# Performance work log

Measured on AMD Instinct MI355X. Metric: run time of the kernel, lower is better.

## Reference

```python
import jax, jax.numpy as jnp
import numpy as np
import math

B, H, M, L, D = 4, 8, 512, 2048, 64   # batch, heads, block len, span, head dim
RAMP = 64                              # adapt_span_len (soft-mask ramp size)


def setup_inputs() -> dict:
    key = jax.random.key(0)
    ks = jax.random.split(key, 5)
    BH = B * H
    KL = M + L
    return {
        "query": jax.random.normal(ks[0], (BH, M, D), jnp.float32),
        "key_": jax.random.normal(ks[1], (BH, KL, D), jnp.float32),
        "value": jax.random.normal(ks[2], (BH, KL, D), jnp.float32),
        "key_pe": jax.random.normal(ks[3], (1, D, L), jnp.float32) * 0.02,
        "current_val": jax.random.uniform(ks[4], (H, 1, 1), jnp.float32, minval=0.3, maxval=0.9),
    }


def reference(query, key_, value, key_pe, current_val):
    BH, Mq, Dh = query.shape
    KL = key_.shape[1]
    Lw = KL - Mq  # attention span
    nb = BH // current_val.shape[0]  # batch size (heads folded into leading dim)

    # full scores then unskew: band[b, i, j] = scores[b, i, i + j]
    scores = jnp.einsum('bmd,bnd->bmn', query, key_)              # (BH, M, M+L)
    rows = jnp.arange(Mq)[:, None]                                # (M, 1)
    band_idx = rows + jnp.arange(Lw)[None, :]                     # (M, L)
    attn = scores[:, rows, band_idx]                              # (BH, M, L)

    # relative position bias, scale, softmax
    attn = attn + jnp.einsum('bmd,dl->bml', query, key_pe[0])
    attn = attn / math.sqrt(Dh)
    attn = jax.nn.softmax(attn, axis=-1)

    # adaptive span soft mask (per head) + renormalization
    template = jnp.arange(1 - Lw, 1, dtype=attn.dtype)            # (L,) = linspace(1-L, 0, L)
    mask = jnp.clip((template + current_val * Lw) / RAMP + 1.0, 0.0, 1.0)  # (H, 1, L)
    attn4 = attn.reshape(nb, -1, Mq, Lw) * mask[None]             # (B, H, M, L)
    attn4 = attn4 / (attn4.sum(-1, keepdims=True) + 1e-8)
    attn = attn4.reshape(BH, Mq, Lw)

    # skew back to (BH, M, M+L) and contract with values
    skewed = jnp.zeros((BH, Mq, KL), attn.dtype).at[:, rows, band_idx].set(attn)
    out = jnp.einsum('bmn,bnd->bmd', skewed, value)               # (BH, M, D)
    return out
```

## Files before the change

### kernel.cpp

```cpp
#include <hip/hip_runtime.h>

typedef _Float16 half_t;
typedef _Float16 half8 __attribute__((ext_vector_type(8)));
typedef _Float16 half4 __attribute__((ext_vector_type(4)));
typedef float f32x4 __attribute__((ext_vector_type(4)));

#define MFMA32(a, b, c) __builtin_amdgcn_mfma_f32_16x16x32_f16((a), (b), (c), 0, 0, 0)
#define MFMA16(a, b, c) __builtin_amdgcn_mfma_f32_16x16x16f16((a), (b), (c), 0, 0, 0)

static constexpr int kM  = 512;
static constexpr int kD  = 64;
static constexpr int kKL = 2560;
static constexpr int kL  = 2048;
static constexpr int WS_QS  = 0;
static constexpr int WS_KB  = 1048576;
static constexpr int WS_VC  = WS_KB + 5242880;
static constexpr int WS_PET = WS_VC + 5242880;
static constexpr int WS_Z   = WS_PET + 131072;

__global__ __launch_bounds__(256) void prep_kernel(const float* __restrict__ q,
    const float* __restrict__ k, const float* __restrict__ v,
    const float* __restrict__ pe, half_t* __restrict__ ws, float* __restrict__ out) {
  __shared__ float ls[64 * 72];
  const int b = blockIdx.x, t = threadIdx.x;
  if (b < 3072) {
    const int i = b * 256 + t;
    const float QS = 0.125f * 1.4426950408889634f;
    const float* src; half_t* dst; float sc;
    if (i < 131072) { src = q + (size_t)i * 8; dst = ws + WS_QS + (size_t)i * 8; sc = QS; }
    else { const int j = i - 131072; src = k + (size_t)j * 8; dst = ws + WS_KB + (size_t)j * 8; sc = 1.0f; }
    const float4 a = ((const float4*)src)[0];
    const float4 bb = ((const float4*)src)[1];
    half_t tt[8];
    tt[0] = (half_t)(a.x * sc);  tt[1] = (half_t)(a.y * sc);
    tt[2] = (half_t)(a.z * sc);  tt[3] = (half_t)(a.w * sc);
    tt[4] = (half_t)(bb.x * sc); tt[5] = (half_t)(bb.y * sc);
    tt[6] = (half_t)(bb.z * sc); tt[7] = (half_t)(bb.w * sc);
    *(int4*)dst = *(int4*)tt;
    return;
  }
  if (b >= 4384) {
    if (b < 4640) {
      float4* o = (float4*)out;
      const int base = (b - 4384) * 1024 + t;
#pragma unroll
      for (int u = 0; u < 4; ++u) o[base + u * 256] = float4{0, 0, 0, 0};
    } else {
      float4* z = (float4*)((float*)(ws + WS_Z));
      const int base = (b - 4640) * 1024 + t;
#pragma unroll
      for (int u = 0; u < 4; ++u) z[base + u * 256] = float4{0, 0, 0, 0};
    }
    return;
  }
  const bool isV = (b < 4352);
  int bh = 0, kt = 0, b3 = 0;
  const float* src; int sstride;
  if (isV) {
    const int b2 = b - 3072;
    bh = b2 / 40; kt = b2 % 40;
    src = v + (size_t)(bh * 2560 + kt * 64) * 64; sstride = 64;
  } else {
    b3 = b - 4352;
    src = pe + (size_t)b3 * 64; sstride = 2048;
  }
  const int rr = t >> 4, cq = (t & 15) * 4;
#pragma unroll
  for (int p = 0; p < 4; ++p) {
    const float4 x = *(const float4*)(src + (size_t)(p * 16 + rr) * sstride + cq);
    *(float4*)(ls + (p * 16 + rr) * 72 + cq) = x;
  }
  __syncthreads();
  const int oc = t >> 2, ch = t & 3;
  half_t tmp[16];
#pragma unroll
  for (int i2 = 0; i2 < 16; ++i2) tmp[i2] = (half_t)ls[(ch * 16 + i2) * 72 + oc];
  half_t* o;
  if (isV) {
    o = ws + WS_VC + (size_t)bh * 163840 + ((kt << 1) + (ch >> 1)) * 2048 + oc * 32 + ((ch & 1) << 4);
  } else {
    o = ws + WS_PET + ((size_t)b3 * 64 + oc) * 64 + ch * 16;
  }
  ((int4*)o)[0] = ((int4*)tmp)[0];
  ((int4*)o)[1] = ((int4*)tmp)[1];
}

__global__ __launch_bounds__(256, 3) void attn_kernel(
    const half_t* __restrict__ ws, const float* __restrict__ cvp,
    float* __restrict__ out, float* __restrict__ zmA) {

  __shared__ __align__(16) char smem[36864];
  half_t* lsh = (half_t*)smem;

  const int tid  = threadIdx.x;
  const int lane = tid & 63;
  const int w    = tid >> 6;
  const int c    = lane & 15;
  const int qd   = lane >> 4;

  const int id = blockIdx.x;
  const int bh = ((id & 7) << 2) | (id >> 8);
  const int mid = (id >> 3) & 31;
  const int mb = mid & 3, sp = mid >> 2;
  const int m0 = mb << 7;
  const int g0   = (sp < 4) ? sp * 9 : 36 + (sp - 4) * 8;
  const int tmax = (sp < 4) ? 9 : 8;

  const float cvl = cvp[bh & 7] * 2048.0f - 2047.0f;
  const float cvO = cvl * 0.015625f + 1.0f;

  const half_t* kb  = ws + WS_KB + (size_t)bh * (kKL * kD);
  const half_t* vcb = ws + WS_VC + (size_t)bh * (kKL * kD);
  const half_t* pet = ws + WS_PET;

  half8 bq0[2], bq1[2];
#pragma unroll
  for (int f = 0; f < 2; ++f) {
    const half_t* qrow = ws + WS_QS + (size_t)(bh * kM + m0 + 32 * w + 16 * f + c) * kD;
    bq0[f] = *(const half8*)(qrow + qd * 8);
    bq1[f] = *(const half8*)(qrow + 32 + qd * 8);
  }

  int4 stgK, stgV;
  auto issueKV = [&](int gg) {
    const int r = tid >> 3, seg = tid & 7;
    const int krow = m0 + (gg << 5) + r;
    stgK = *(const int4*)(kb + (size_t)krow * kD + seg * 8);
    const int vch = (m0 >> 5) + gg;
    stgV = *(const int4*)(vcb + (size_t)vch * 2048 + tid * 8);
  };
  auto commitKV = [&](int gg) {
    const int sK = (gg & 1) * 2304;
    const int sV = 4608 + (gg & 1) * 2560;
    const int r = tid >> 3, seg = tid & 7;
    *(int4*)(lsh + sK + r * 72 + seg * 8) = stgK;
    const int d = tid >> 2, ks = (tid & 3) * 8;
    *(int4*)(lsh + sV + d * 40 + ks) = stgV;
  };

  auto stripWrite = [&](int f, int wb, const f32x4& a) {
    half_t* stf = lsh + 9728 + (w * 2 + f) * 1088 + c * 68;
    const int allone  = (wb >= 0) && (wb + 15 <= kL - 1) && (wb + cvl >= 0.0f);
    const int allzero = (wb > kL - 1) || (wb + 15 < 0) || ((float)(wb + 15) + cvl <= -64.0f);
#pragma unroll
    for (int reg = 0; reg < 4; ++reg) {
      const int l = wb + qd * 4 + reg;
      const float bt = a[reg] * 0.6931472f;
      float e = __builtin_fmaf(bt, 0.16666667f, 0.5f);
      e = __builtin_fmaf(e, bt, 1.0f);
      e = __builtin_fmaf(e, bt, 1.0f);
      float em;
      if (allzero) em = 0.0f;
      else if (allone) em = e;
      else {
        const float mk = fminf(fmaxf((float)l * 0.015625f + cvO, 0.0f), 1.0f);
        em = ((unsigned)l < (unsigned)kL) ? e * mk : 0.0f;
      }
      stf[(l + c) & 63] = (half_t)em;
    }
  };
  auto peWindow = [&](int wb, f32x4& accf0, f32x4& accf1, bool dof0, bool dof1) {
    int l = wb + c; l = l < 0 ? 0 : (l > kL - 1 ? kL - 1 : l);
    const half8 p0 = *(const half8*)(pet + (size_t)l * kD + qd * 8);
    const half8 p1 = *(const half8*)(pet + (size_t)l * kD + 32 + qd * 8);
    if (dof0) { f32x4 a = {0,0,0,0}; a = MFMA32(p0, bq0[0], a); accf0 = MFMA32(p1, bq1[0], a); }
    if (dof1) { f32x4 a = {0,0,0,0}; a = MFMA32(p0, bq0[1], a); accf1 = MFMA32(p1, bq1[1], a); }
  };

  issueKV(g0);
  const int B0 = (g0 << 5) - 32 * w;
#pragma unroll
  for (int k4 = 0; k4 < 4; ++k4) {
    const int wb = B0 + 16 - (k4 << 4);
    f32x4 a0, a1;
    const bool d0 = (k4 <= 2), d1 = (k4 >= 1);
    peWindow(wb, a0, a1, d0, d1);
    if (d0) stripWrite(0, wb, a0);
    if (d1) stripWrite(1, wb, a1);
  }
  commitKV(g0);
  __syncthreads();

  float zmc[2] = {0, 0};
  f32x4 o[2][4];
#pragma unroll
  for (int f = 0; f < 2; ++f)
#pragma unroll
    for (int dc = 0; dc < 4; ++dc) o[f][dc] = f32x4{0, 0, 0, 0};

  for (int t = 0; t < tmax; ++t) {
    const int g = g0 + t;
    const bool more = (t + 1 < tmax);
    if (more) issueKV(g + 1);

    const int sK = (g & 1) * 2304;
    const int sV = 4608 + (g & 1) * 2560;
    const int B = (g << 5) - 32 * w;

    const half8 ak00 = *(const half8*)(lsh + sK + c * 72 + qd * 8);
    const half8 ak01 = *(const half8*)(lsh + sK + c * 72 + 32 + qd * 8);
    const half8 ak10 = *(const half8*)(lsh + sK + (16 + c) * 72 + qd * 8);
    const half8 ak11 = *(const half8*)(lsh + sK + (16 + c) * 72 + 32 + qd * 8);

#pragma unroll
    for (int f = 0; f < 2; ++f) {
      f32x4 s0 = {0, 0, 0, 0}, s1 = {0, 0, 0, 0};
      s0 = MFMA32(ak00, bq0[f], s0); s0 = MFMA32(ak01, bq1[f], s0);
      s1 = MFMA32(ak10, bq0[f], s1); s1 = MFMA32(ak11, bq1[f], s1);

      const int base_f = B - 16 * f;
      const half_t* stf = lsh + 9728 + (w * 2 + f) * 1088 + c * 68;
      const half4 em0 = *(const half4*)(stf + ((base_f + qd * 4) & 63));
      const half4 em1 = *(const half4*)(stf + ((base_f + 16 + qd * 4) & 63));

      float pm0[4], pm1[4];
#pragma unroll
      for (int reg = 0; reg < 4; ++reg) {
        pm0[reg] = __builtin_amdgcn_exp2f(s0[reg]) * (float)em0[reg];
        pm1[reg] = __builtin_amdgcn_exp2f(s1[reg]) * (float)em1[reg];
        zmc[f] += pm0[reg] + pm1[reg];
      }
      const half4 pb0h = { (half_t)pm0[0], (half_t)pm0[1], (half_t)pm0[2], (half_t)pm0[3] };
      const half4 pb1h = { (half_t)pm1[0], (half_t)pm1[1], (half_t)pm1[2], (half_t)pm1[3] };
#pragma unroll
      for (int dc = 0; dc < 4; ++dc) {
        const half4 av0 = *(const half4*)(lsh + sV + (dc * 16 + c) * 40 + qd * 4);
        const half4 av1 = *(const half4*)(lsh + sV + (dc * 16 + c) * 40 + 16 + qd * 4);
        o[f][dc] = MFMA16(av0, pb0h, o[f][dc]);
        o[f][dc] = MFMA16(av1, pb1h, o[f][dc]);
      }
    }

    if (more) {
#pragma unroll
      for (int k3 = 0; k3 < 3; ++k3) {
        const int wb = B + 48 - (k3 << 4);
        f32x4 a0, a1;
        const bool d0 = (k3 <= 1), d1 = (k3 >= 1);
        peWindow(wb, a0, a1, d0, d1);
        if (d0) stripWrite(0, wb, a0);
        if (d1) stripWrite(1, wb, a1);
      }
      commitKV(g + 1);
    }
    __syncthreads();
  }

  __syncthreads();
  float* Ow = (float*)smem + (size_t)w * 2176;
#pragma unroll
  for (int f = 0; f < 2; ++f)
#pragma unroll
    for (int dc = 0; dc < 4; ++dc)
      *(f32x4*)(Ow + (16 * f + c) * 68 + dc * 16 + qd * 4) = o[f][dc];

#pragma unroll
  for (int f = 0; f < 2; ++f) {
    float m = zmc[f];
    m += __shfl_xor(m, 16); m += __shfl_xor(m, 32);
    if (lane < 16) {
      const int row = bh * kM + m0 + 32 * w + 16 * f + c;
      atomicAdd(&zmA[row], m);
    }
  }
  const int rowbase = bh * kM + m0 + 32 * w;
  for (int rr = 0; rr < 32; ++rr)
    atomicAdd(out + (size_t)(rowbase + rr) * kD + lane, Ow[rr * 68 + lane]);
}

__global__ __launch_bounds__(256) void norm_kernel(const float* __restrict__ zmA,
    float* __restrict__ out) {
  const int i = blockIdx.x * 256 + threadIdx.x;
  const int row = i >> 4, d4 = (i & 15) << 2;
  const float inv = 1.0f / (zmA[row] + 1e-20f);
  float4* p = (float4*)(out + (size_t)row * 64 + d4);
  float4 v = *p;
  v.x *= inv; v.y *= inv; v.z *= inv; v.w *= inv;
  *p = v;
}

extern "C" void kernel_launch(void* const* d_in, const int* in_sizes, int n_in,
                              void* d_out, int out_size, void* d_ws, size_t ws_size,
                              hipStream_t stream) {
  (void)in_sizes; (void)n_in; (void)out_size; (void)ws_size;
  const float* q  = (const float*)d_in[0];
  const float* k  = (const float*)d_in[1];
  const float* v  = (const float*)d_in[2];
  const float* pe = (const float*)d_in[3];
  const float* cv = (const float*)d_in[4];
  half_t* ws = (half_t*)d_ws;
  float* out = (float*)d_out;
  float* zmA = (float*)(ws + WS_Z);

  prep_kernel<<<4648, 256, 0, stream>>>(q, k, v, pe, ws, out);
  attn_kernel<<<1024, 256, 0, stream>>>(ws, cv, out, zmA);
  norm_kernel<<<1024, 256, 0, stream>>>(zmA, out);
}
```

Before: 153.1 us.

## Use 8 waves of 16 query rows per block and split KV loads across waves

Blocks of the attention kernel now have 512 threads (8 waves), each handling 16 query rows instead of 32. The grid changes from 1024 to 768 blocks with 6 span splits of 11–12 groups per 128-row tile. K and V staging is split so half the waves load K and the other half load V. The aim is more wavefronts per CU with fewer registers per wave, fewer span partitions and so fewer output atomics, and a larger tile per block. In exchange, K/V tiles are reused across fewer query rows per wave, and each block has 8 waves to synchronise.

```diff
diff --git a/kernel.cpp b/kernel.cpp
--- a/kernel.cpp
+++ b/kernel.cpp
@@ -85,7 +85,7 @@
   ((int4*)o)[1] = ((int4*)tmp)[1];
 }
 
-__global__ __launch_bounds__(256, 3) void attn_kernel(
+__global__ __launch_bounds__(512, 6) void attn_kernel(
     const half_t* __restrict__ ws, const float* __restrict__ cvp,
     float* __restrict__ out, float* __restrict__ zmA) {
 
@@ -99,12 +99,14 @@
   const int qd   = lane >> 4;
 
   const int id = blockIdx.x;
-  const int bh = ((id & 7) << 2) | (id >> 8);
-  const int mid = (id >> 3) & 31;
-  const int mb = mid & 3, sp = mid >> 2;
+  const int x  = id & 7;
+  const int y  = id >> 3;
+  const int bh = (x << 2) | (y / 24);
+  const int r2 = y % 24;
+  const int mb = r2 / 6, sp = r2 % 6;
   const int m0 = mb << 7;
-  const int g0   = (sp < 4) ? sp * 9 : 36 + (sp - 4) * 8;
-  const int tmax = (sp < 4) ? 9 : 8;
+  const int g0   = (sp < 2) ? sp * 12 : 24 + (sp - 2) * 11;
+  const int tmax = (sp < 2) ? 12 : 11;
 
   const float cvl = cvp[bh & 7] * 2048.0f - 2047.0f;
   const float cvO = cvl * 0.015625f + 1.0f;
@@ -113,33 +115,37 @@
   const half_t* vcb = ws + WS_VC + (size_t)bh * (kKL * kD);
   const half_t* pet = ws + WS_PET;
 
-  half8 bq0[2], bq1[2];
-#pragma unroll
-  for (int f = 0; f < 2; ++f) {
-    const half_t* qrow = ws + WS_QS + (size_t)(bh * kM + m0 + 32 * w + 16 * f + c) * kD;
-    bq0[f] = *(const half8*)(qrow + qd * 8);
-    bq1[f] = *(const half8*)(qrow + 32 + qd * 8);
-  }
-
-  int4 stgK, stgV;
+  const half_t* qrow = ws + WS_QS + (size_t)(bh * kM + m0 + 16 * w + c) * kD;
+  const half8 bq0 = *(const half8*)(qrow + qd * 8);
+  const half8 bq1 = *(const half8*)(qrow + 32 + qd * 8);
+
+  int4 stg;
   auto issueKV = [&](int gg) {
-    const int r = tid >> 3, seg = tid & 7;
-    const int krow = m0 + (gg << 5) + r;
-    stgK = *(const int4*)(kb + (size_t)krow * kD + seg * 8);
-    const int vch = (m0 >> 5) + gg;
-    stgV = *(const int4*)(vcb + (size_t)vch * 2048 + tid * 8);
+    if (w < 4) {
+      const int r = tid >> 3, seg = tid & 7;
+      const int krow = m0 + (gg << 5) + r;
+      stg = *(const int4*)(kb + (size_t)krow * kD + seg * 8);
+    } else {
+      const int i = tid - 256;
+      const int vch = (m0 >> 5) + gg;
+      stg = *(const int4*)(vcb + (size_t)vch * 2048 + i * 8);
+    }
   };
   auto commitKV = [&](int gg) {
-    const int sK = (gg & 1) * 2304;
-    const int sV = 4608 + (gg & 1) * 2560;
-    const int r = tid >> 3, seg = tid & 7;
-    *(int4*)(lsh + sK + r * 72 + seg * 8) = stgK;
-    const int d = tid >> 2, ks = (tid & 3) * 8;
-    *(int4*)(lsh + sV + d * 40 + ks) = stgV;
-  };
-
-  auto stripWrite = [&](int f, int wb, const f32x4& a) {
-    half_t* stf = lsh + 9728 + (w * 2 + f) * 1088 + c * 68;
+    if (w < 4) {
+      const int sK = (gg & 1) * 2304;
+      const int r = tid >> 3, seg = tid & 7;
+      *(int4*)(lsh + sK + r * 72 + seg * 8) = stg;
+    } else {
+      const int sV = 4608 + (gg & 1) * 2560;
+      const int i = tid - 256;
+      const int d = i >> 2, ks = (i & 3) * 8;
+      *(int4*)(lsh + sV + d * 40 + ks) = stg;
+    }
+  };
+
+  half_t* stf = lsh + 9728 + w * 1088 + c * 68;
+  auto stripWrite = [&](int wb, const f32x4& a) {
     const int allone  = (wb >= 0) && (wb + 15 <= kL - 1) && (wb + cvl >= 0.0f);
     const int allzero = (wb > kL - 1) || (wb + 15 < 0) || ((float)(wb + 15) + cvl <= -64.0f);
 #pragma unroll
@@ -159,34 +165,27 @@
       stf[(l + c) & 63] = (half_t)em;
     }
   };
-  auto peWindow = [&](int wb, f32x4& accf0, f32x4& accf1, bool dof0, bool dof1) {
+  auto peWindow = [&](int wb) -> f32x4 {
     int l = wb + c; l = l < 0 ? 0 : (l > kL - 1 ? kL - 1 : l);
     const half8 p0 = *(const half8*)(pet + (size_t)l * kD + qd * 8);
     const half8 p1 = *(const half8*)(pet + (size_t)l * kD + 32 + qd * 8);
-    if (dof0) { f32x4 a = {0,0,0,0}; a = MFMA32(p0, bq0[0], a); accf0 = MFMA32(p1, bq1[0], a); }
-    if (dof1) { f32x4 a = {0,0,0,0}; a = MFMA32(p0, bq0[1], a); accf1 = MFMA32(p1, bq1[1], a); }
+    f32x4 a = {0, 0, 0, 0};
+    a = MFMA32(p0, bq0, a);
+    return MFMA32(p1, bq1, a);
   };
 
   issueKV(g0);
-  const int B0 = (g0 << 5) - 32 * w;
-#pragma unroll
-  for (int k4 = 0; k4 < 4; ++k4) {
-    const int wb = B0 + 16 - (k4 << 4);
-    f32x4 a0, a1;
-    const bool d0 = (k4 <= 2), d1 = (k4 >= 1);
-    peWindow(wb, a0, a1, d0, d1);
-    if (d0) stripWrite(0, wb, a0);
-    if (d1) stripWrite(1, wb, a1);
+  const int B0 = (g0 << 5) - 16 * w;
+#pragma unroll
+  for (int k3 = 0; k3 < 3; ++k3) {
+    const int wb = B0 - 16 + (k3 << 4);
+    stripWrite(wb, peWindow(wb));
   }
   commitKV(g0);
   __syncthreads();
 
-  float zmc[2] = {0, 0};
-  f32x4 o[2][4];
-#pragma unroll
-  for (int f = 0; f < 2; ++f)
-#pragma unroll
-    for (int dc = 0; dc < 4; ++dc) o[f][dc] = f32x4{0, 0, 0, 0};
+  float zmc = 0.0f;
+  f32x4 o0 = {0,0,0,0}, o1 = {0,0,0,0}, o2 = {0,0,0,0}, o3 = {0,0,0,0};
 
   for (int t = 0; t < tmax; ++t) {
     const int g = g0 + t;
@@ -195,76 +194,62 @@
 
     const int sK = (g & 1) * 2304;
     const int sV = 4608 + (g & 1) * 2560;
-    const int B = (g << 5) - 32 * w;
+    const int base = (g << 5) - 16 * w;
 
     const half8 ak00 = *(const half8*)(lsh + sK + c * 72 + qd * 8);
     const half8 ak01 = *(const half8*)(lsh + sK + c * 72 + 32 + qd * 8);
     const half8 ak10 = *(const half8*)(lsh + sK + (16 + c) * 72 + qd * 8);
     const half8 ak11 = *(const half8*)(lsh + sK + (16 + c) * 72 + 32 + qd * 8);
 
-#pragma unroll
-    for (int f = 0; f < 2; ++f) {
-      f32x4 s0 = {0, 0, 0, 0}, s1 = {0, 0, 0, 0};
-      s0 = MFMA32(ak00, bq0[f], s0); s0 = MFMA32(ak01, bq1[f], s0);
-      s1 = MFMA32(ak10, bq0[f], s1); s1 = MFMA32(ak11, bq1[f], s1);
-
-      const int base_f = B - 16 * f;
-      const half_t* stf = lsh + 9728 + (w * 2 + f) * 1088 + c * 68;
-      const half4 em0 = *(const half4*)(stf + ((base_f + qd * 4) & 63));
-      const half4 em1 = *(const half4*)(stf + ((base_f + 16 + qd * 4) & 63));
-
-      float pm0[4], pm1[4];
-#pragma unroll
-      for (int reg = 0; reg < 4; ++reg) {
-        pm0[reg] = __builtin_amdgcn_exp2f(s0[reg]) * (float)em0[reg];
-        pm1[reg] = __builtin_amdgcn_exp2f(s1[reg]) * (float)em1[reg];
-        zmc[f] += pm0[reg] + pm1[reg];
-      }
-      const half4 pb0h = { (half_t)pm0[0], (half_t)pm0[1], (half_t)pm0[2], (half_t)pm0[3] };
-      const half4 pb1h = { (half_t)pm1[0], (half_t)pm1[1], (half_t)pm1[2], (half_t)pm1[3] };
-#pragma unroll
-      for (int dc = 0; dc < 4; ++dc) {
-        const half4 av0 = *(const half4*)(lsh + sV + (dc * 16 + c) * 40 + qd * 4);
-        const half4 av1 = *(const half4*)(lsh + sV + (dc * 16 + c) * 40 + 16 + qd * 4);
-        o[f][dc] = MFMA16(av0, pb0h, o[f][dc]);
-        o[f][dc] = MFMA16(av1, pb1h, o[f][dc]);
-      }
+    f32x4 s0 = {0, 0, 0, 0}, s1 = {0, 0, 0, 0};
+    s0 = MFMA32(ak00, bq0, s0); s0 = MFMA32(ak01, bq1, s0);
+    s1 = MFMA32(ak10, bq0, s1); s1 = MFMA32(ak11, bq1, s1);
+
+    const half4 em0 = *(const half4*)(stf + ((base + qd * 4) & 63));
+    const half4 em1 = *(const half4*)(stf + ((base + 16 + qd * 4) & 63));
+
+    float pm0[4], pm1[4];
+#pragma unroll
+    for (int reg = 0; reg < 4; ++reg) {
+      pm0[reg] = __builtin_amdgcn_exp2f(s0[reg]) * (float)em0[reg];
+      pm1[reg] = __builtin_amdgcn_exp2f(s1[reg]) * (float)em1[reg];
+      zmc += pm0[reg] + pm1[reg];
+    }
+    const half4 pb0h = { (half_t)pm0[0], (half_t)pm0[1], (half_t)pm0[2], (half_t)pm0[3] };
+    const half4 pb1h = { (half_t)pm1[0], (half_t)pm1[1], (half_t)pm1[2], (half_t)pm1[3] };
+#pragma unroll
+    for (int dc = 0; dc < 4; ++dc) {
+      const half4 av0 = *(const half4*)(lsh + sV + (dc * 16 + c) * 40 + qd * 4);
+      const half4 av1 = *(const half4*)(lsh + sV + (dc * 16 + c) * 40 + 16 + qd * 4);
+      f32x4& od = (dc == 0) ? o0 : (dc == 1) ? o1 : (dc == 2) ? o2 : o3;
+      od = MFMA16(av0, pb0h, od);
+      od = MFMA16(av1, pb1h, od);
     }
 
     if (more) {
-#pragma unroll
-      for (int k3 = 0; k3 < 3; ++k3) {
-        const int wb = B + 48 - (k3 << 4);
-        f32x4 a0, a1;
-        const bool d0 = (k3 <= 1), d1 = (k3 >= 1);
-        peWindow(wb, a0, a1, d0, d1);
-        if (d0) stripWrite(0, wb, a0);
-        if (d1) stripWrite(1, wb, a1);
-      }
+      const int wb1 = base + 32, wb2 = base + 48;
+      stripWrite(wb1, peWindow(wb1));
+      stripWrite(wb2, peWindow(wb2));
       commitKV(g + 1);
     }
     __syncthreads();
   }
 
   __syncthreads();
-  float* Ow = (float*)smem + (size_t)w * 2176;
-#pragma unroll
-  for (int f = 0; f < 2; ++f)
-#pragma unroll
-    for (int dc = 0; dc < 4; ++dc)
-      *(f32x4*)(Ow + (16 * f + c) * 68 + dc * 16 + qd * 4) = o[f][dc];
-
-#pragma unroll
-  for (int f = 0; f < 2; ++f) {
-    float m = zmc[f];
-    m += __shfl_xor(m, 16); m += __shfl_xor(m, 32);
-    if (lane < 16) {
-      const int row = bh * kM + m0 + 32 * w + 16 * f + c;
-      atomicAdd(&zmA[row], m);
-    }
-  }
-  const int rowbase = bh * kM + m0 + 32 * w;
-  for (int rr = 0; rr < 32; ++rr)
+  float* Ow = (float*)smem + (size_t)w * 1088;
+  *(f32x4*)(Ow + c * 68 + 0  + qd * 4) = o0;
+  *(f32x4*)(Ow + c * 68 + 16 + qd * 4) = o1;
+  *(f32x4*)(Ow + c * 68 + 32 + qd * 4) = o2;
+  *(f32x4*)(Ow + c * 68 + 48 + qd * 4) = o3;
+
+  float m = zmc;
+  m += __shfl_xor(m, 16); m += __shfl_xor(m, 32);
+  if (lane < 16) {
+    const int row = bh * kM + m0 + 16 * w + c;
+    atomicAdd(&zmA[row], m);
+  }
+  const int rowbase = bh * kM + m0 + 16 * w;
+  for (int rr = 0; rr < 16; ++rr)
     atomicAdd(out + (size_t)(rowbase + rr) * kD + lane, Ow[rr * 68 + lane]);
 }
 
@@ -293,6 +278,6 @@
   float* zmA = (float*)(ws + WS_Z);
 
   prep_kernel<<<4648, 256, 0, stream>>>(q, k, v, pe, ws, out);
-  attn_kernel<<<1024, 256, 0, stream>>>(ws, cv, out, zmA);
+  attn_kernel<<<768, 512, 0, stream>>>(ws, cv, out, zmA);
   norm_kernel<<<1024, 256, 0, stream>>>(zmA, out);
 }
```

New measurement: 147.7 us. 3.6% less time.

## Switch attention to 32x32x16 MFMA tiles and halve grid with longer span splits

Applied to the files above, without the earlier changes.

Replaces the 16x16 MFMA score, positional-bias and PV products with 32x32x16 MFMA instructions over whole 32-row strips per wave. The score-to-P transpose now goes through a per-wave LDS scratch buffer. The span is split into 4 chunks of 17 steps instead of 8, so the grid is 512 blocks at 2 blocks/CU occupancy. The aim is fewer MFMA issues, fewer atomics and less per-block prologue, at the cost of lower parallelism, more LDS and extra LDS round trips.

```diff
diff --git a/kernel.cpp b/kernel.cpp
--- a/kernel.cpp
+++ b/kernel.cpp
@@ -4,9 +4,9 @@
 typedef _Float16 half8 __attribute__((ext_vector_type(8)));
 typedef _Float16 half4 __attribute__((ext_vector_type(4)));
 typedef float f32x4 __attribute__((ext_vector_type(4)));
-
-#define MFMA32(a, b, c) __builtin_amdgcn_mfma_f32_16x16x32_f16((a), (b), (c), 0, 0, 0)
-#define MFMA16(a, b, c) __builtin_amdgcn_mfma_f32_16x16x16f16((a), (b), (c), 0, 0, 0)
+typedef float f32x16 __attribute__((ext_vector_type(16)));
+
+#define MFMA_S(a, b, c) __builtin_amdgcn_mfma_f32_32x32x16_f16((a), (b), (c), 0, 0, 0)
 
 static constexpr int kM  = 512;
 static constexpr int kD  = 64;
@@ -85,26 +85,25 @@
   ((int4*)o)[1] = ((int4*)tmp)[1];
 }
 
-__global__ __launch_bounds__(256, 3) void attn_kernel(
+__global__ __launch_bounds__(256, 2) void attn_kernel(
     const half_t* __restrict__ ws, const float* __restrict__ cvp,
     float* __restrict__ out, float* __restrict__ zmA) {
 
-  __shared__ __align__(16) char smem[36864];
+  __shared__ __align__(16) char smem[47104];
   half_t* lsh = (half_t*)smem;
 
   const int tid  = threadIdx.x;
   const int lane = tid & 63;
   const int w    = tid >> 6;
-  const int c    = lane & 15;
-  const int qd   = lane >> 4;
+  const int c32  = lane & 31;
+  const int h    = lane >> 5;
 
   const int id = blockIdx.x;
-  const int bh = ((id & 7) << 2) | (id >> 8);
-  const int mid = (id >> 3) & 31;
+  const int bh = ((id & 7) << 2) | (id >> 7);
+  const int mid = (id >> 3) & 15;
   const int mb = mid & 3, sp = mid >> 2;
   const int m0 = mb << 7;
-  const int g0   = (sp < 4) ? sp * 9 : 36 + (sp - 4) * 8;
-  const int tmax = (sp < 4) ? 9 : 8;
+  const int g0 = sp * 17;
 
   const float cvl = cvp[bh & 7] * 2048.0f - 2047.0f;
   const float cvO = cvl * 0.015625f + 1.0f;
@@ -113,13 +112,13 @@
   const half_t* vcb = ws + WS_VC + (size_t)bh * (kKL * kD);
   const half_t* pet = ws + WS_PET;
 
-  half8 bq0[2], bq1[2];
-#pragma unroll
-  for (int f = 0; f < 2; ++f) {
-    const half_t* qrow = ws + WS_QS + (size_t)(bh * kM + m0 + 32 * w + 16 * f + c) * kD;
-    bq0[f] = *(const half8*)(qrow + qd * 8);
-    bq1[f] = *(const half8*)(qrow + 32 + qd * 8);
-  }
+  const half_t* qrow = ws + WS_QS + (size_t)(bh * kM + m0 + 32 * w + c32) * kD;
+  half8 bq[4];
+#pragma unroll
+  for (int t = 0; t < 4; ++t) bq[t] = *(const half8*)(qrow + t * 16 + h * 8);
+
+  half_t* stf = lsh + 9728 + w * 2176 + c32 * 68;
+  half_t* pw  = lsh + 18432 + w * 1280;
 
   int4 stgK, stgV;
   auto issueKV = [&](int gg) {
@@ -138,13 +137,24 @@
     *(int4*)(lsh + sV + d * 40 + ks) = stgV;
   };
 
-  auto stripWrite = [&](int f, int wb, const f32x4& a) {
-    half_t* stf = lsh + 9728 + (w * 2 + f) * 1088 + c * 68;
-    const int allone  = (wb >= 0) && (wb + 15 <= kL - 1) && (wb + cvl >= 0.0f);
-    const int allzero = (wb > kL - 1) || (wb + 15 < 0) || ((float)(wb + 15) + cvl <= -64.0f);
-#pragma unroll
-    for (int reg = 0; reg < 4; ++reg) {
-      const int l = wb + qd * 4 + reg;
+  auto peWindow = [&](int wb) -> f32x16 {
+    int l = wb + c32; l = l < 0 ? 0 : (l > kL - 1 ? kL - 1 : l);
+    const half_t* pp = pet + (size_t)l * kD;
+    f32x16 a = {};
+#pragma unroll
+    for (int t = 0; t < 4; ++t) {
+      const half8 p = *(const half8*)(pp + t * 16 + h * 8);
+      a = MFMA_S(p, bq[t], a);
+    }
+    return a;
+  };
+  auto stripWrite = [&](int wb, const f32x16& a) {
+    const int allone  = (wb >= 0) && (wb + 31 <= kL - 1) && (wb + cvl >= 0.0f);
+    const int allzero = (wb > kL - 1) || (wb + 31 < 0) || ((float)(wb + 31) + cvl <= -64.0f);
+#pragma unroll
+    for (int reg = 0; reg < 16; ++reg) {
+      const int lr = (reg & 3) + 8 * (reg >> 2) + 4 * h;
+      const int l  = wb + lr;
       const float bt = a[reg] * 0.6931472f;
       float e = __builtin_fmaf(bt, 0.16666667f, 0.5f);
       e = __builtin_fmaf(e, bt, 1.0f);
@@ -156,91 +166,72 @@
         const float mk = fminf(fmaxf((float)l * 0.015625f + cvO, 0.0f), 1.0f);
         em = ((unsigned)l < (unsigned)kL) ? e * mk : 0.0f;
       }
-      stf[(l + c) & 63] = (half_t)em;
-    }
-  };
-  auto peWindow = [&](int wb, f32x4& accf0, f32x4& accf1, bool dof0, bool dof1) {
-    int l = wb + c; l = l < 0 ? 0 : (l > kL - 1 ? kL - 1 : l);
-    const half8 p0 = *(const half8*)(pet + (size_t)l * kD + qd * 8);
-    const half8 p1 = *(const half8*)(pet + (size_t)l * kD + 32 + qd * 8);
-    if (dof0) { f32x4 a = {0,0,0,0}; a = MFMA32(p0, bq0[0], a); accf0 = MFMA32(p1, bq1[0], a); }
-    if (dof1) { f32x4 a = {0,0,0,0}; a = MFMA32(p0, bq0[1], a); accf1 = MFMA32(p1, bq1[1], a); }
+      stf[(l + c32) & 63] = (half_t)em;
+    }
   };
 
   issueKV(g0);
   const int B0 = (g0 << 5) - 32 * w;
-#pragma unroll
-  for (int k4 = 0; k4 < 4; ++k4) {
-    const int wb = B0 + 16 - (k4 << 4);
-    f32x4 a0, a1;
-    const bool d0 = (k4 <= 2), d1 = (k4 >= 1);
-    peWindow(wb, a0, a1, d0, d1);
-    if (d0) stripWrite(0, wb, a0);
-    if (d1) stripWrite(1, wb, a1);
-  }
+  stripWrite(B0 - 32, peWindow(B0 - 32));
+  stripWrite(B0,      peWindow(B0));
   commitKV(g0);
   __syncthreads();
 
-  float zmc[2] = {0, 0};
-  f32x4 o[2][4];
-#pragma unroll
-  for (int f = 0; f < 2; ++f)
-#pragma unroll
-    for (int dc = 0; dc < 4; ++dc) o[f][dc] = f32x4{0, 0, 0, 0};
-
-  for (int t = 0; t < tmax; ++t) {
+  float zmc = 0.0f;
+  f32x16 o0 = {}, o1 = {};
+
+  for (int t = 0; t < 17; ++t) {
     const int g = g0 + t;
-    const bool more = (t + 1 < tmax);
+    const bool more = (t < 16);
     if (more) issueKV(g + 1);
 
     const int sK = (g & 1) * 2304;
     const int sV = 4608 + (g & 1) * 2560;
     const int B = (g << 5) - 32 * w;
 
-    const half8 ak00 = *(const half8*)(lsh + sK + c * 72 + qd * 8);
-    const half8 ak01 = *(const half8*)(lsh + sK + c * 72 + 32 + qd * 8);
-    const half8 ak10 = *(const half8*)(lsh + sK + (16 + c) * 72 + qd * 8);
-    const half8 ak11 = *(const half8*)(lsh + sK + (16 + c) * 72 + 32 + qd * 8);
-
-#pragma unroll
-    for (int f = 0; f < 2; ++f) {
-      f32x4 s0 = {0, 0, 0, 0}, s1 = {0, 0, 0, 0};
-      s0 = MFMA32(ak00, bq0[f], s0); s0 = MFMA32(ak01, bq1[f], s0);
-      s1 = MFMA32(ak10, bq0[f], s1); s1 = MFMA32(ak11, bq1[f], s1);
-
-      const int base_f = B - 16 * f;
-      const half_t* stf = lsh + 9728 + (w * 2 + f) * 1088 + c * 68;
-      const half4 em0 = *(const half4*)(stf + ((base_f + qd * 4) & 63));
-      const half4 em1 = *(const half4*)(stf + ((base_f + 16 + qd * 4) & 63));
-
-      float pm0[4], pm1[4];
-#pragma unroll
-      for (int reg = 0; reg < 4; ++reg) {
-        pm0[reg] = __builtin_amdgcn_exp2f(s0[reg]) * (float)em0[reg];
-        pm1[reg] = __builtin_amdgcn_exp2f(s1[reg]) * (float)em1[reg];
-        zmc[f] += pm0[reg] + pm1[reg];
-      }
-      const half4 pb0h = { (half_t)pm0[0], (half_t)pm0[1], (half_t)pm0[2], (half_t)pm0[3] };
-      const half4 pb1h = { (half_t)pm1[0], (half_t)pm1[1], (half_t)pm1[2], (half_t)pm1[3] };
-#pragma unroll
-      for (int dc = 0; dc < 4; ++dc) {
-        const half4 av0 = *(const half4*)(lsh + sV + (dc * 16 + c) * 40 + qd * 4);
-        const half4 av1 = *(const half4*)(lsh + sV + (dc * 16 + c) * 40 + 16 + qd * 4);
-        o[f][dc] = MFMA16(av0, pb0h, o[f][dc]);
-        o[f][dc] = MFMA16(av1, pb1h, o[f][dc]);
-      }
-    }
+    half8 ak[4];
+#pragma unroll
+    for (int kt = 0; kt < 4; ++kt)
+      ak[kt] = *(const half8*)(lsh + sK + c32 * 72 + kt * 16 + h * 8);
+
+    half4 emq[4];
+#pragma unroll
+    for (int q = 0; q < 4; ++q)
+      emq[q] = *(const half4*)(stf + ((B + 8 * q + 4 * h) & 63));
+
+    half8 av[2][2];
+#pragma unroll
+    for (int dh = 0; dh < 2; ++dh)
+#pragma unroll
+      for (int kt = 0; kt < 2; ++kt)
+        av[dh][kt] = *(const half8*)(lsh + sV + (32 * dh + c32) * 40 + kt * 16 + h * 8);
+
+    f32x16 s = {};
+#pragma unroll
+    for (int kt = 0; kt < 4; ++kt) s = MFMA_S(ak[kt], bq[kt], s);
+
+    float pm[16];
+#pragma unroll
+    for (int reg = 0; reg < 16; ++reg) {
+      pm[reg] = __builtin_amdgcn_exp2f(s[reg]) * (float)emq[reg >> 2][reg & 3];
+      zmc += pm[reg];
+    }
+#pragma unroll
+    for (int q = 0; q < 4; ++q) {
+      const half4 pq = { (half_t)pm[q * 4], (half_t)pm[q * 4 + 1],
+                         (half_t)pm[q * 4 + 2], (half_t)pm[q * 4 + 3] };
+      *(half4*)(pw + c32 * 40 + 8 * q + 4 * h) = pq;
+    }
+
+    const half8 pb0 = *(const half8*)(pw + c32 * 40 + 0  + h * 8);
+    const half8 pb1 = *(const half8*)(pw + c32 * 40 + 16 + h * 8);
+    o0 = MFMA_S(av[0][0], pb0, o0);
+    o0 = MFMA_S(av[0][1], pb1, o0);
+    o1 = MFMA_S(av[1][0], pb0, o1);
+    o1 = MFMA_S(av[1][1], pb1, o1);
 
     if (more) {
-#pragma unroll
-      for (int k3 = 0; k3 < 3; ++k3) {
-        const int wb = B + 48 - (k3 << 4);
-        f32x4 a0, a1;
-        const bool d0 = (k3 <= 1), d1 = (k3 >= 1);
-        peWindow(wb, a0, a1, d0, d1);
-        if (d0) stripWrite(0, wb, a0);
-        if (d1) stripWrite(1, wb, a1);
-      }
+      stripWrite(B + 32, peWindow(B + 32));
       commitKV(g + 1);
     }
     __syncthreads();
@@ -249,19 +240,16 @@
   __syncthreads();
   float* Ow = (float*)smem + (size_t)w * 2176;
 #pragma unroll
-  for (int f = 0; f < 2; ++f)
-#pragma unroll
-    for (int dc = 0; dc < 4; ++dc)
-      *(f32x4*)(Ow + (16 * f + c) * 68 + dc * 16 + qd * 4) = o[f][dc];
-
-#pragma unroll
-  for (int f = 0; f < 2; ++f) {
-    float m = zmc[f];
-    m += __shfl_xor(m, 16); m += __shfl_xor(m, 32);
-    if (lane < 16) {
-      const int row = bh * kM + m0 + 32 * w + 16 * f + c;
-      atomicAdd(&zmA[row], m);
-    }
+  for (int q = 0; q < 4; ++q) {
+    *(f32x4*)(Ow + c32 * 68 + 0  + 8 * q + 4 * h) =
+        f32x4{o0[q * 4], o0[q * 4 + 1], o0[q * 4 + 2], o0[q * 4 + 3]};
+    *(f32x4*)(Ow + c32 * 68 + 32 + 8 * q + 4 * h) =
+        f32x4{o1[q * 4], o1[q * 4 + 1], o1[q * 4 + 2], o1[q * 4 + 3]};
+  }
+  zmc += __shfl_xor(zmc, 32);
+  if (lane < 32) {
+    const int row = bh * kM + m0 + 32 * w + c32;
+    atomicAdd(&zmA[row], zmc);
   }
   const int rowbase = bh * kM + m0 + 32 * w;
   for (int rr = 0; rr < 32; ++rr)
@@ -293,6 +281,6 @@
   float* zmA = (float*)(ws + WS_Z);
 
   prep_kernel<<<4648, 256, 0, stream>>>(q, k, v, pe, ws, out);
-  attn_kernel<<<1024, 256, 0, stream>>>(ws, cv, out, zmA);
+  attn_kernel<<<512, 256, 0, stream>>>(ws, cv, out, zmA);
   norm_kernel<<<1024, 256, 0, stream>>>(zmA, out);
 }
```

Result: faster. 137.4 us (-10.3%).
